# Performance work log

Measured on AMD Instinct MI355X. Metric: run time of the kernel, lower is better.

## Reference

```python
import jax, jax.numpy as jnp
import numpy as np

B, NC, N, DN, ALPHA = 8, 64, 128, 64, 2
HS, HM, HMOD = 256, 256, 64
STATE_IN, MSG_IN = 3 * DN, 2 * DN
MOD_IN = 2 * DN + 5
MOD_OUT = N * N + N


def _u(key, shape, fan_in):
    # kaiming_uniform-like init
    bound = 1.0 / np.sqrt(fan_in)
    return jax.random.uniform(key, shape, jnp.float32, -bound, bound)


def setup_inputs() -> dict:
    key = jax.random.key(0)
    ks = jax.random.split(key, 24)
    f = jnp.float32
    return {
        'h': jax.random.normal(ks[0], (B, NC, N, DN), f) * 0.01,
        'msg': jax.random.normal(ks[1], (B, NC, N, DN), f) * 0.01,
        'W': jax.random.normal(ks[2], (B, NC, N, N), f) * 0.05,
        'decay_logit': jnp.zeros((B, NC, N), f),
        'readout_drift': jnp.zeros((B, NC, 1), f),
        's_mem_live': jnp.zeros((B,), f),
        's_mem_ema_fast': jnp.zeros((B,), f),
        'H_aug_t': jax.random.normal(ks[3], (B, NC * DN), f),
        'neuron_id': jax.random.normal(ks[4], (NC, N, DN), f) * 0.02,
        'state_w1': _u(ks[5], (HS, STATE_IN), STATE_IN),
        'state_b1': jnp.zeros((HS,), f),
        'state_w2': _u(ks[6], (DN, HS), HS) * 0.1,
        'state_b2': jnp.zeros((DN,), f),
        'msg_w1': _u(ks[7], (HM, MSG_IN), MSG_IN),
        'msg_b1': jnp.zeros((HM,), f),
        'msg_w2': _u(ks[8], (DN, HM), HM) * 0.1,
        'msg_b2': jnp.zeros((DN,), f),
        'inject_w': _u(ks[9], (NC, ALPHA * DN, DN), DN),
        'inject_b': jnp.zeros((NC, ALPHA * DN), f),
        'mod_w1': _u(ks[10], (NC, MOD_IN, HMOD), HMOD),
        'mod_b1': jnp.zeros((NC, HMOD), f),
        'mod_w2': _u(ks[11], (NC, HMOD, MOD_OUT), MOD_OUT) * 0.01,
        'mod_b2': jnp.zeros((NC, MOD_OUT), f),
    }


def _mlp2(x, w1, b1, w2, b2):
    # F.linear -> tanh -> F.linear -> tanh
    hid = jnp.tanh(jnp.einsum('...i,hi->...h', x, w1) + b1)
    return jnp.tanh(jnp.einsum('...h,oh->...o', hid, w2) + b2)


def reference(h, msg, W, decay_logit, readout_drift, s_mem_live, s_mem_ema_fast,
              H_aug_t, neuron_id, state_w1, state_b1, state_w2, state_b2,
              msg_w1, msg_b1, msg_w2, msg_b2, inject_w, inject_b,
              mod_w1, mod_b1, mod_w2, mod_b2):
    # --- message passing: received = W @ msg  [B,NC,N,DN] ---
    received = jnp.einsum('bcij,bcjd->bcid', W, msg)

    # --- inject external input into the first ALPHA (input) neurons ---
    cell_slice = H_aug_t.reshape(B, NC, DN)               # [B,NC,DN]
    inject = jnp.einsum('bni,noi->bno', cell_slice, inject_w) + inject_b[None]
    inject = inject.reshape(B, NC, ALPHA, DN)
    received = received.at[:, :, :ALPHA].add(inject)

    # --- state update MLP (shared across cells/neurons) ---
    nid = jnp.broadcast_to(neuron_id[None], (B, NC, N, DN))
    state_in = jnp.concatenate([h, received, nid], axis=-1)      # [B,NC,N,3*DN]
    h_new = _mlp2(state_in, state_w1, state_b1, state_w2, state_b2)

    # --- message MLP ---
    msg_in = jnp.concatenate([h_new, received], axis=-1)         # [B,NC,N,2*DN]
    msg_new = _mlp2(msg_in, msg_w1, msg_b1, msg_w2, msg_b2)

    # --- modulator input (per _build_mod_input) ---
    h_mean = h_new.mean(axis=2)                                  # [B,NC,DN]
    msg_mean = msg_new.mean(axis=2)                              # [B,NC,DN]
    W_stats = jnp.abs(W).mean(axis=-1).mean(axis=2, keepdims=True)  # [B,NC,1]
    decay_mean = decay_logit.mean(axis=2, keepdims=True)         # [B,NC,1]
    s1 = jnp.broadcast_to(s_mem_live[:, None, None], (B, NC, 1))
    s2 = jnp.broadcast_to(s_mem_ema_fast[:, None, None], (B, NC, 1))
    mod_input = jnp.concatenate(
        [h_mean, msg_mean, W_stats, decay_mean, readout_drift, s1, s2], axis=-1)

    # --- per-cell modulator MLP (per _modulator_forward) ---
    hidden = jnp.tanh(jnp.einsum('bni,nih->bnh', mod_input, mod_w1) + mod_b1[None])
    mod_out = jnp.einsum('bnh,nho->bno', hidden, mod_w2) + mod_b2[None]

    # --- apply modulator action to recurrent adjacency + decay ---
    delta_W = mod_out[..., :N * N].reshape(B, NC, N, N)
    delta_decay = mod_out[..., N * N:N * N + N].reshape(B, NC, N)
    W_new = W + delta_W
    decay_new = decay_logit + delta_decay
    return (h_new, msg_new, W_new, decay_new)
```

## Files before the change

### kernel.cpp

```cpp
#include <hip/hip_runtime.h>
#include <hip/hip_bf16.h>
#include <math.h>


typedef __bf16 bf16_t;
typedef __attribute__((ext_vector_type(8))) __bf16 bf16x8;
typedef __attribute__((ext_vector_type(4))) float f32x4;

__device__ __forceinline__ float fast_tanh(float x) {
  float e = __expf(2.0f * x);
  return 1.0f - 2.0f / (e + 1.0f);
}

__device__ __forceinline__ f32x4 mfma16(bf16x8 a, bf16x8 b, f32x4 c) {
  return __builtin_amdgcn_mfma_f32_16x16x32_bf16(a, b, c, 0, 0, 0);
}

__device__ __forceinline__ bf16x8 ldcvt8(const float* p) {
  f32x4 a = *(const f32x4*)p;
  f32x4 b = *(const f32x4*)(p + 4);
  bf16x8 o;
#pragma unroll
  for (int u = 0; u < 4; ++u) { o[u] = (bf16_t)a[u]; o[u + 4] = (bf16_t)b[u]; }
  return o;
}

__global__ __launch_bounds__(256) void k_convert(
    const float* __restrict__ sw1, const float* __restrict__ sw2,
    const float* __restrict__ mw1, const float* __restrict__ mw2,
    bf16_t* __restrict__ out) {
  int i = blockIdx.x * 256 + threadIdx.x;
  float v;
  if (i < 49152) v = sw1[i];
  else if (i < 65536) v = sw2[i - 49152];
  else if (i < 98304) v = mw1[i - 65536];
  else v = mw2[i - 98304];
  out[i] = (bf16_t)v;
}

__global__ __launch_bounds__(256) void k_fused(
    const float* __restrict__ W, const float* __restrict__ msg,
    const float* __restrict__ h, const float* __restrict__ nid,
    const float* __restrict__ Haug, const float* __restrict__ injw,
    const float* __restrict__ injb, const bf16_t* __restrict__ wbf,
    const float* __restrict__ sb1, const float* __restrict__ sb2,
    const float* __restrict__ msb1, const float* __restrict__ msb2,
    const float* __restrict__ decay, const float* __restrict__ rdrift,
    const float* __restrict__ sml, const float* __restrict__ smf,
    const float* __restrict__ mw1, const float* __restrict__ mb1,
    float* __restrict__ out_h, float* __restrict__ out_m,
    float* __restrict__ hidden) {
  int bc = blockIdx.x, c = bc & 63, b = bc >> 6;
  __shared__ bf16_t Mt[64][136];
  __shared__ bf16_t recs[128][72];
  __shared__ bf16_t hs[128][72];
  __shared__ bf16_t hnew[128][72];
  __shared__ float inj[128];
  __shared__ float hsum[4][64];
  __shared__ float msum[4][64];
  __shared__ float wsum[4];
  __shared__ float modin[133];
  int t = threadIdx.x;

  const float* Mp = msg + (size_t)bc * 8192;
  for (int s = 0; s < 8; ++s) {
    int e = (s * 256 + t) * 4;
    f32x4 v = *(const f32x4*)(Mp + e);
    int j = e >> 6, d = e & 63;
#pragma unroll
    for (int u = 0; u < 4; ++u) Mt[d + u][j] = (bf16_t)v[u];
  }
  if (t < 128) {
    const float* cell = Haug + (size_t)b * 4096 + c * 64;
    const float* iw = injw + (size_t)c * 8192 + t * 64;
    float a = injb[c * 128 + t];
    for (int k = 0; k < 64; ++k) a += cell[k] * iw[k];
    inj[t] = a;
  }
  __syncthreads();

  int wave = t >> 6, l = t & 63, lr = l & 15, kg = l >> 4;
  int r0 = wave * 32;

  const float* Wp = W + (size_t)bc * 16384;
  float asum = 0.f;
  f32x4 racc[2][4] = {};
#pragma unroll
  for (int ks = 0; ks < 4; ++ks) {
    int kof = ks * 32 + kg * 8;
    const float* p0 = Wp + (size_t)(r0 + lr) * 128 + kof;
    const float* p1 = Wp + (size_t)(r0 + 16 + lr) * 128 + kof;
    f32x4 x0 = *(const f32x4*)p0, x1 = *(const f32x4*)(p0 + 4);
    f32x4 y0 = *(const f32x4*)p1, y1 = *(const f32x4*)(p1 + 4);
    bf16x8 a0, a1;
#pragma unroll
    for (int u = 0; u < 4; ++u) {
      a0[u] = (bf16_t)x0[u]; a0[u + 4] = (bf16_t)x1[u];
      a1[u] = (bf16_t)y0[u]; a1[u + 4] = (bf16_t)y1[u];
      asum += fabsf(x0[u]) + fabsf(x1[u]) + fabsf(y0[u]) + fabsf(y1[u]);
    }
#pragma unroll
    for (int ni = 0; ni < 4; ++ni) {
      bf16x8 bfr = *(const bf16x8*)&Mt[ni * 16 + lr][kof];
      racc[0][ni] = mfma16(a0, bfr, racc[0][ni]);
      racc[1][ni] = mfma16(a1, bfr, racc[1][ni]);
    }
  }
#pragma unroll
  for (int mi = 0; mi < 2; ++mi)
#pragma unroll
    for (int ni = 0; ni < 4; ++ni)
#pragma unroll
      for (int r = 0; r < 4; ++r) {
        int row = r0 + mi * 16 + kg * 4 + r, col = ni * 16 + lr;
        float v = racc[mi][ni][r];
        if (row < 2) v += inj[row * 64 + col];
        recs[row][col] = (bf16_t)v;
      }

  const float* hp = h + (size_t)bc * 8192;
  const float* np2 = nid + (size_t)c * 8192;
  bf16x8 aA[2][6];
#pragma unroll
  for (int mi = 0; mi < 2; ++mi) {
    int row = r0 + mi * 16 + lr;
#pragma unroll
    for (int ks = 0; ks < 6; ++ks) {
      int kof = ks * 32 + kg * 8;
      if (ks < 2)      aA[mi][ks] = ldcvt8(hp + (size_t)row * 64 + kof);
      else if (ks < 4) aA[mi][ks] = *(const bf16x8*)&recs[row][kof - 64];
      else             aA[mi][ks] = ldcvt8(np2 + (size_t)row * 64 + (kof - 128));
    }
  }
  const bf16_t* w1b = wbf;
  const bf16_t* w2b = wbf + 49152;
  const bf16_t* w3b = wbf + 65536;
  const bf16_t* w4b = wbf + 98304;
  f32x4 acc2[2][4] = {};
  for (int hc = 0; hc < 4; ++hc) {
    f32x4 a1[2][4] = {};
#pragma unroll
    for (int ks = 0; ks < 6; ++ks) {
      int kof = ks * 32 + kg * 8;
#pragma unroll
      for (int ni = 0; ni < 4; ++ni) {
        bf16x8 bfr = *(const bf16x8*)(w1b + (size_t)(hc * 64 + ni * 16 + lr) * 192 + kof);
        a1[0][ni] = mfma16(aA[0][ks], bfr, a1[0][ni]);
        a1[1][ni] = mfma16(aA[1][ks], bfr, a1[1][ni]);
      }
    }
#pragma unroll
    for (int mi = 0; mi < 2; ++mi)
#pragma unroll
      for (int ni = 0; ni < 4; ++ni) {
        float bias = sb1[hc * 64 + ni * 16 + lr];
#pragma unroll
        for (int r = 0; r < 4; ++r)
          hs[r0 + mi * 16 + kg * 4 + r][ni * 16 + lr] = (bf16_t)fast_tanh(a1[mi][ni][r] + bias);
      }
#pragma unroll
    for (int ks = 0; ks < 2; ++ks) {
      int kof = ks * 32 + kg * 8;
      bf16x8 af0 = *(const bf16x8*)&hs[r0 + lr][kof];
      bf16x8 af1 = *(const bf16x8*)&hs[r0 + 16 + lr][kof];
#pragma unroll
      for (int ni = 0; ni < 4; ++ni) {
        bf16x8 bfr = *(const bf16x8*)(w2b + (size_t)(ni * 16 + lr) * 256 + hc * 64 + kof);
        acc2[0][ni] = mfma16(af0, bfr, acc2[0][ni]);
        acc2[1][ni] = mfma16(af1, bfr, acc2[1][ni]);
      }
    }
  }
  float* ohp = out_h + (size_t)bc * 8192;
  float hpart[4] = {0.f, 0.f, 0.f, 0.f};
#pragma unroll
  for (int mi = 0; mi < 2; ++mi)
#pragma unroll
    for (int ni = 0; ni < 4; ++ni) {
      float bias = sb2[ni * 16 + lr];
#pragma unroll
      for (int r = 0; r < 4; ++r) {
        int row = r0 + mi * 16 + kg * 4 + r, col = ni * 16 + lr;
        float v = fast_tanh(acc2[mi][ni][r] + bias);
        ohp[row * 64 + col] = v;
        hnew[row][col] = (bf16_t)v;
        hpart[ni] += v;
      }
    }
#pragma unroll
  for (int ni = 0; ni < 4; ++ni) {
    float s = hpart[ni];
    s += __shfl_xor(s, 16);
    s += __shfl_xor(s, 32);
    if (l < 16) hsum[wave][ni * 16 + l] = s;
  }

  bf16x8 aB[2][4];
#pragma unroll
  for (int mi = 0; mi < 2; ++mi) {
    int row = r0 + mi * 16 + lr;
#pragma unroll
    for (int ks = 0; ks < 4; ++ks) {
      int kof = ks * 32 + kg * 8;
      if (ks < 2) aB[mi][ks] = *(const bf16x8*)&hnew[row][kof];
      else        aB[mi][ks] = *(const bf16x8*)&recs[row][kof - 64];
    }
  }
  f32x4 acc3[2][4] = {};
  for (int hc = 0; hc < 4; ++hc) {
    f32x4 g3[2][4] = {};
#pragma unroll
    for (int ks = 0; ks < 4; ++ks) {
      int kof = ks * 32 + kg * 8;
#pragma unroll
      for (int ni = 0; ni < 4; ++ni) {
        bf16x8 bfr = *(const bf16x8*)(w3b + (size_t)(hc * 64 + ni * 16 + lr) * 128 + kof);
        g3[0][ni] = mfma16(aB[0][ks], bfr, g3[0][ni]);
        g3[1][ni] = mfma16(aB[1][ks], bfr, g3[1][ni]);
      }
    }
#pragma unroll
    for (int mi = 0; mi < 2; ++mi)
#pragma unroll
      for (int ni = 0; ni < 4; ++ni) {
        float bias = msb1[hc * 64 + ni * 16 + lr];
#pragma unroll
        for (int r = 0; r < 4; ++r)
          hs[r0 + mi * 16 + kg * 4 + r][ni * 16 + lr] = (bf16_t)fast_tanh(g3[mi][ni][r] + bias);
      }
#pragma unroll
    for (int ks = 0; ks < 2; ++ks) {
      int kof = ks * 32 + kg * 8;
      bf16x8 af0 = *(const bf16x8*)&hs[r0 + lr][kof];
      bf16x8 af1 = *(const bf16x8*)&hs[r0 + 16 + lr][kof];
#pragma unroll
      for (int ni = 0; ni < 4; ++ni) {
        bf16x8 bfr = *(const bf16x8*)(w4b + (size_t)(ni * 16 + lr) * 256 + hc * 64 + kof);
        acc3[0][ni] = mfma16(af0, bfr, acc3[0][ni]);
        acc3[1][ni] = mfma16(af1, bfr, acc3[1][ni]);
      }
    }
  }
  float* omp = out_m + (size_t)bc * 8192;
  float mpart[4] = {0.f, 0.f, 0.f, 0.f};
#pragma unroll
  for (int mi = 0; mi < 2; ++mi)
#pragma unroll
    for (int ni = 0; ni < 4; ++ni) {
      float bias = msb2[ni * 16 + lr];
#pragma unroll
      for (int r = 0; r < 4; ++r) {
        int row = r0 + mi * 16 + kg * 4 + r, col = ni * 16 + lr;
        float v = fast_tanh(acc3[mi][ni][r] + bias);
        omp[row * 64 + col] = v;
        mpart[ni] += v;
      }
    }
#pragma unroll
  for (int ni = 0; ni < 4; ++ni) {
    float s = mpart[ni];
    s += __shfl_xor(s, 16);
    s += __shfl_xor(s, 32);
    if (l < 16) msum[wave][ni * 16 + l] = s;
  }
  {
    float s = asum;
#pragma unroll
    for (int off = 32; off > 0; off >>= 1) s += __shfl_xor(s, off);
    if (l == 0) wsum[wave] = s;
  }
  if (wave == 3) {
    float s = decay[(size_t)bc * 128 + l] + decay[(size_t)bc * 128 + 64 + l];
#pragma unroll
    for (int off = 32; off > 0; off >>= 1) s += __shfl_xor(s, off);
    if (l == 0) modin[129] = s * (1.f / 128.f);
  }
  __syncthreads();

  if (t < 64)
    modin[t] = (hsum[0][t] + hsum[1][t] + hsum[2][t] + hsum[3][t]) * (1.f / 128.f);
  else if (t < 128) {
    int d = t - 64;
    modin[64 + d] = (msum[0][d] + msum[1][d] + msum[2][d] + msum[3][d]) * (1.f / 128.f);
  } else if (t == 128)
    modin[128] = (wsum[0] + wsum[1] + wsum[2] + wsum[3]) * (1.f / 16384.f);
  else if (t == 130) modin[130] = rdrift[bc];
  else if (t == 131) modin[131] = sml[b];
  else if (t == 132) modin[132] = smf[b];
  __syncthreads();

  if (t < 64) {
    const float* w = mw1 + (size_t)c * 133 * 64;
    float a = mb1[c * 64 + t];
    for (int i = 0; i < 133; ++i) a += modin[i] * w[i * 64 + t];
    hidden[((size_t)(c * 64 + t)) * 8 + b] = fast_tanh(a);
  }
}

__global__ __launch_bounds__(256) void k_apply(
    const float* __restrict__ hidden, const float* __restrict__ mw2,
    const float* __restrict__ mb2, const float* __restrict__ W,
    const float* __restrict__ decay, float* __restrict__ out_W,
    float* __restrict__ out_d) {
  int c = blockIdx.y, ch = blockIdx.x, t = threadIdx.x;
  int o = ch * 1024 + t * 4;
  if (o >= 16512) return;
  const float* w2 = mw2 + (size_t)c * 64 * 16512 + o;
  const float* hq = hidden + (size_t)c * 512;
  f32x4 bias = *(const f32x4*)(mb2 + (size_t)c * 16512 + o);
  f32x4 acc[8];
#pragma unroll
  for (int b = 0; b < 8; ++b) acc[b] = bias;
  for (int hh = 0; hh < 64; ++hh) {
    f32x4 wv = __builtin_nontemporal_load((const f32x4*)(w2 + (size_t)hh * 16512));
    f32x4 h0 = *(const f32x4*)(hq + hh * 8);
    f32x4 h1 = *(const f32x4*)(hq + hh * 8 + 4);
#pragma unroll
    for (int b = 0; b < 4; ++b) { acc[b] += h0[b] * wv; acc[b + 4] += h1[b] * wv; }
  }
  if (o < 16384) {
#pragma unroll
    for (int b = 0; b < 8; ++b) {
      size_t idx = (size_t)(b * 64 + c) * 16384 + o;
      f32x4 wv = *(const f32x4*)(W + idx);
      __builtin_nontemporal_store(wv + acc[b], (f32x4*)(out_W + idx));
    }
  } else {
    int i = o - 16384;
#pragma unroll
    for (int b = 0; b < 8; ++b) {
      size_t idx = (size_t)(b * 64 + c) * 128 + i;
      f32x4 dv = *(const f32x4*)(decay + idx);
      __builtin_nontemporal_store(dv + acc[b], (f32x4*)(out_d + idx));
    }
  }
}

extern "C" void kernel_launch(void* const* d_in, const int* in_sizes, int n_in,
                              void* d_out, int out_size, void* d_ws, size_t ws_size,
                              hipStream_t stream) {
  const float* h = (const float*)d_in[0];
  const float* msg = (const float*)d_in[1];
  const float* W = (const float*)d_in[2];
  const float* decay = (const float*)d_in[3];
  const float* rdrift = (const float*)d_in[4];
  const float* sml = (const float*)d_in[5];
  const float* smf = (const float*)d_in[6];
  const float* Haug = (const float*)d_in[7];
  const float* nid = (const float*)d_in[8];
  const float* sw1 = (const float*)d_in[9];
  const float* sb1 = (const float*)d_in[10];
  const float* sw2 = (const float*)d_in[11];
  const float* sb2 = (const float*)d_in[12];
  const float* mw1 = (const float*)d_in[13];
  const float* mb1 = (const float*)d_in[14];
  const float* mw2 = (const float*)d_in[15];
  const float* mb2 = (const float*)d_in[16];
  const float* injw = (const float*)d_in[17];
  const float* injb = (const float*)d_in[18];
  const float* modw1 = (const float*)d_in[19];
  const float* modb1 = (const float*)d_in[20];
  const float* modw2 = (const float*)d_in[21];
  const float* modb2 = (const float*)d_in[22];

  float* out = (float*)d_out;
  float* out_h = out;
  float* out_m = out + 4194304;
  float* out_W = out + 8388608;
  float* out_d = out + 16777216;

  char* wsb = (char*)d_ws;
  bf16_t* wbf = (bf16_t*)wsb;
  float* hidden = (float*)(wsb + 262144);

  k_convert<<<448, 256, 0, stream>>>(sw1, sw2, mw1, mw2, wbf);
  k_fused<<<512, 256, 0, stream>>>(W, msg, h, nid, Haug, injw, injb, wbf,
                                   sb1, sb2, mb1, mb2, decay, rdrift, sml, smf,
                                   modw1, modb1, out_h, out_m, hidden);
  k_apply<<<dim3(17, 64), 256, 0, stream>>>(hidden, modw2, modb2, W, decay, out_W, out_d);
}
```

Baseline: 535.1 us.

## Split fused kernel rows across eight waves and stage modulator hidden in LDS

The fused per-cell kernel now runs 512 threads in eight waves, each owning 16 rows instead of 32. This halves the accumulators per wave and should allow more waves in flight to hide latency. The h, neuron_id and decay loads are hoisted above the first barrier, and the inject dot product is vectorised. The apply kernel stages the per-cell hidden vector in shared memory rather than rereading it from global memory on every iteration. The cost is that each wave now fetches the bf16 MLP weights for only 16 rows, so weight traffic per MFMA roughly doubles.

Result: slower. 561.0 us (+4.8%).

```diff
diff --git a/kernel.cpp b/kernel.cpp
--- a/kernel.cpp
+++ b/kernel.cpp
@@ -38,7 +38,7 @@
   out[i] = (bf16_t)v;
 }
 
-__global__ __launch_bounds__(256) void k_fused(
+__global__ __launch_bounds__(512, 4) void k_fused(
     const float* __restrict__ W, const float* __restrict__ msg,
     const float* __restrict__ h, const float* __restrict__ nid,
     const float* __restrict__ Haug, const float* __restrict__ injw,
@@ -56,15 +56,17 @@
   __shared__ bf16_t hs[128][72];
   __shared__ bf16_t hnew[128][72];
   __shared__ float inj[128];
-  __shared__ float hsum[4][64];
-  __shared__ float msum[4][64];
-  __shared__ float wsum[4];
+  __shared__ float hsum[8][64];
+  __shared__ float msum[8][64];
+  __shared__ float wsum[8];
   __shared__ float modin[133];
   int t = threadIdx.x;
+  int wave = t >> 6, l = t & 63, lr = l & 15, kg = l >> 4;
+  int r0 = wave * 16;
 
   const float* Mp = msg + (size_t)bc * 8192;
-  for (int s = 0; s < 8; ++s) {
-    int e = (s * 256 + t) * 4;
+  for (int s = 0; s < 4; ++s) {
+    int e = (s * 512 + t) * 4;
     f32x4 v = *(const f32x4*)(Mp + e);
     int j = e >> 6, d = e & 63;
 #pragma unroll
@@ -74,119 +76,108 @@
     const float* cell = Haug + (size_t)b * 4096 + c * 64;
     const float* iw = injw + (size_t)c * 8192 + t * 64;
     float a = injb[c * 128 + t];
-    for (int k = 0; k < 64; ++k) a += cell[k] * iw[k];
+    for (int k = 0; k < 64; k += 4) {
+      f32x4 w4 = *(const f32x4*)(iw + k);
+      a += cell[k] * w4[0] + cell[k + 1] * w4[1] + cell[k + 2] * w4[2] + cell[k + 3] * w4[3];
+    }
     inj[t] = a;
   }
+
+  const float* hp = h + (size_t)bc * 8192;
+  const float* np2 = nid + (size_t)c * 8192;
+  int arow = r0 + lr;
+  bf16x8 aA[6];
+  aA[0] = ldcvt8(hp + (size_t)arow * 64 + kg * 8);
+  aA[1] = ldcvt8(hp + (size_t)arow * 64 + 32 + kg * 8);
+  aA[4] = ldcvt8(np2 + (size_t)arow * 64 + kg * 8);
+  aA[5] = ldcvt8(np2 + (size_t)arow * 64 + 32 + kg * 8);
+  float dv0 = 0.f, dv1 = 0.f;
+  if (wave == 7) {
+    dv0 = decay[(size_t)bc * 128 + l];
+    dv1 = decay[(size_t)bc * 128 + 64 + l];
+  }
   __syncthreads();
-
-  int wave = t >> 6, l = t & 63, lr = l & 15, kg = l >> 4;
-  int r0 = wave * 32;
 
   const float* Wp = W + (size_t)bc * 16384;
   float asum = 0.f;
-  f32x4 racc[2][4] = {};
+  f32x4 racc[4] = {};
 #pragma unroll
   for (int ks = 0; ks < 4; ++ks) {
     int kof = ks * 32 + kg * 8;
-    const float* p0 = Wp + (size_t)(r0 + lr) * 128 + kof;
-    const float* p1 = Wp + (size_t)(r0 + 16 + lr) * 128 + kof;
+    const float* p0 = Wp + (size_t)arow * 128 + kof;
     f32x4 x0 = *(const f32x4*)p0, x1 = *(const f32x4*)(p0 + 4);
-    f32x4 y0 = *(const f32x4*)p1, y1 = *(const f32x4*)(p1 + 4);
-    bf16x8 a0, a1;
+    bf16x8 a0;
 #pragma unroll
     for (int u = 0; u < 4; ++u) {
       a0[u] = (bf16_t)x0[u]; a0[u + 4] = (bf16_t)x1[u];
-      a1[u] = (bf16_t)y0[u]; a1[u + 4] = (bf16_t)y1[u];
-      asum += fabsf(x0[u]) + fabsf(x1[u]) + fabsf(y0[u]) + fabsf(y1[u]);
+      asum += fabsf(x0[u]) + fabsf(x1[u]);
     }
 #pragma unroll
     for (int ni = 0; ni < 4; ++ni) {
       bf16x8 bfr = *(const bf16x8*)&Mt[ni * 16 + lr][kof];
-      racc[0][ni] = mfma16(a0, bfr, racc[0][ni]);
-      racc[1][ni] = mfma16(a1, bfr, racc[1][ni]);
-    }
-  }
-#pragma unroll
-  for (int mi = 0; mi < 2; ++mi)
-#pragma unroll
-    for (int ni = 0; ni < 4; ++ni)
-#pragma unroll
-      for (int r = 0; r < 4; ++r) {
-        int row = r0 + mi * 16 + kg * 4 + r, col = ni * 16 + lr;
-        float v = racc[mi][ni][r];
-        if (row < 2) v += inj[row * 64 + col];
-        recs[row][col] = (bf16_t)v;
-      }
-
-  const float* hp = h + (size_t)bc * 8192;
-  const float* np2 = nid + (size_t)c * 8192;
-  bf16x8 aA[2][6];
-#pragma unroll
-  for (int mi = 0; mi < 2; ++mi) {
-    int row = r0 + mi * 16 + lr;
-#pragma unroll
-    for (int ks = 0; ks < 6; ++ks) {
-      int kof = ks * 32 + kg * 8;
-      if (ks < 2)      aA[mi][ks] = ldcvt8(hp + (size_t)row * 64 + kof);
-      else if (ks < 4) aA[mi][ks] = *(const bf16x8*)&recs[row][kof - 64];
-      else             aA[mi][ks] = ldcvt8(np2 + (size_t)row * 64 + (kof - 128));
-    }
-  }
+      racc[ni] = mfma16(a0, bfr, racc[ni]);
+    }
+  }
+#pragma unroll
+  for (int ni = 0; ni < 4; ++ni)
+#pragma unroll
+    for (int r = 0; r < 4; ++r) {
+      int row = r0 + kg * 4 + r, col = ni * 16 + lr;
+      float v = racc[ni][r];
+      if (row < 2) v += inj[row * 64 + col];
+      recs[row][col] = (bf16_t)v;
+    }
+
+  aA[2] = *(const bf16x8*)&recs[arow][kg * 8];
+  aA[3] = *(const bf16x8*)&recs[arow][32 + kg * 8];
   const bf16_t* w1b = wbf;
   const bf16_t* w2b = wbf + 49152;
   const bf16_t* w3b = wbf + 65536;
   const bf16_t* w4b = wbf + 98304;
-  f32x4 acc2[2][4] = {};
+  f32x4 acc2[4] = {};
   for (int hc = 0; hc < 4; ++hc) {
-    f32x4 a1[2][4] = {};
+    f32x4 a1[4] = {};
 #pragma unroll
     for (int ks = 0; ks < 6; ++ks) {
       int kof = ks * 32 + kg * 8;
 #pragma unroll
       for (int ni = 0; ni < 4; ++ni) {
         bf16x8 bfr = *(const bf16x8*)(w1b + (size_t)(hc * 64 + ni * 16 + lr) * 192 + kof);
-        a1[0][ni] = mfma16(aA[0][ks], bfr, a1[0][ni]);
-        a1[1][ni] = mfma16(aA[1][ks], bfr, a1[1][ni]);
+        a1[ni] = mfma16(aA[ks], bfr, a1[ni]);
       }
     }
 #pragma unroll
-    for (int mi = 0; mi < 2; ++mi)
-#pragma unroll
-      for (int ni = 0; ni < 4; ++ni) {
-        float bias = sb1[hc * 64 + ni * 16 + lr];
-#pragma unroll
-        for (int r = 0; r < 4; ++r)
-          hs[r0 + mi * 16 + kg * 4 + r][ni * 16 + lr] = (bf16_t)fast_tanh(a1[mi][ni][r] + bias);
-      }
+    for (int ni = 0; ni < 4; ++ni) {
+      float bias = sb1[hc * 64 + ni * 16 + lr];
+#pragma unroll
+      for (int r = 0; r < 4; ++r)
+        hs[r0 + kg * 4 + r][ni * 16 + lr] = (bf16_t)fast_tanh(a1[ni][r] + bias);
+    }
 #pragma unroll
     for (int ks = 0; ks < 2; ++ks) {
       int kof = ks * 32 + kg * 8;
-      bf16x8 af0 = *(const bf16x8*)&hs[r0 + lr][kof];
-      bf16x8 af1 = *(const bf16x8*)&hs[r0 + 16 + lr][kof];
+      bf16x8 af = *(const bf16x8*)&hs[arow][kof];
 #pragma unroll
       for (int ni = 0; ni < 4; ++ni) {
         bf16x8 bfr = *(const bf16x8*)(w2b + (size_t)(ni * 16 + lr) * 256 + hc * 64 + kof);
-        acc2[0][ni] = mfma16(af0, bfr, acc2[0][ni]);
-        acc2[1][ni] = mfma16(af1, bfr, acc2[1][ni]);
+        acc2[ni] = mfma16(af, bfr, acc2[ni]);
       }
     }
   }
   float* ohp = out_h + (size_t)bc * 8192;
   float hpart[4] = {0.f, 0.f, 0.f, 0.f};
 #pragma unroll
-  for (int mi = 0; mi < 2; ++mi)
-#pragma unroll
-    for (int ni = 0; ni < 4; ++ni) {
-      float bias = sb2[ni * 16 + lr];
-#pragma unroll
-      for (int r = 0; r < 4; ++r) {
-        int row = r0 + mi * 16 + kg * 4 + r, col = ni * 16 + lr;
-        float v = fast_tanh(acc2[mi][ni][r] + bias);
-        ohp[row * 64 + col] = v;
-        hnew[row][col] = (bf16_t)v;
-        hpart[ni] += v;
-      }
-    }
+  for (int ni = 0; ni < 4; ++ni) {
+    float bias = sb2[ni * 16 + lr];
+#pragma unroll
+    for (int r = 0; r < 4; ++r) {
+      int row = r0 + kg * 4 + r, col = ni * 16 + lr;
+      float v = fast_tanh(acc2[ni][r] + bias);
+      ohp[row * 64 + col] = v;
+      hnew[row][col] = (bf16_t)v;
+      hpart[ni] += v;
+    }
+  }
 #pragma unroll
   for (int ni = 0; ni < 4; ++ni) {
     float s = hpart[ni];
@@ -195,67 +186,54 @@
     if (l < 16) hsum[wave][ni * 16 + l] = s;
   }
 
-  bf16x8 aB[2][4];
-#pragma unroll
-  for (int mi = 0; mi < 2; ++mi) {
-    int row = r0 + mi * 16 + lr;
+  bf16x8 aB[4];
+  aB[0] = *(const bf16x8*)&hnew[arow][kg * 8];
+  aB[1] = *(const bf16x8*)&hnew[arow][32 + kg * 8];
+  aB[2] = aA[2];
+  aB[3] = aA[3];
+  f32x4 acc3[4] = {};
+  for (int hc = 0; hc < 4; ++hc) {
+    f32x4 g3[4] = {};
 #pragma unroll
     for (int ks = 0; ks < 4; ++ks) {
       int kof = ks * 32 + kg * 8;
-      if (ks < 2) aB[mi][ks] = *(const bf16x8*)&hnew[row][kof];
-      else        aB[mi][ks] = *(const bf16x8*)&recs[row][kof - 64];
-    }
-  }
-  f32x4 acc3[2][4] = {};
-  for (int hc = 0; hc < 4; ++hc) {
-    f32x4 g3[2][4] = {};
-#pragma unroll
-    for (int ks = 0; ks < 4; ++ks) {
-      int kof = ks * 32 + kg * 8;
 #pragma unroll
       for (int ni = 0; ni < 4; ++ni) {
         bf16x8 bfr = *(const bf16x8*)(w3b + (size_t)(hc * 64 + ni * 16 + lr) * 128 + kof);
-        g3[0][ni] = mfma16(aB[0][ks], bfr, g3[0][ni]);
-        g3[1][ni] = mfma16(aB[1][ks], bfr, g3[1][ni]);
+        g3[ni] = mfma16(aB[ks], bfr, g3[ni]);
       }
     }
 #pragma unroll
-    for (int mi = 0; mi < 2; ++mi)
-#pragma unroll
-      for (int ni = 0; ni < 4; ++ni) {
-        float bias = msb1[hc * 64 + ni * 16 + lr];
-#pragma unroll
-        for (int r = 0; r < 4; ++r)
-          hs[r0 + mi * 16 + kg * 4 + r][ni * 16 + lr] = (bf16_t)fast_tanh(g3[mi][ni][r] + bias);
-      }
+    for (int ni = 0; ni < 4; ++ni) {
+      float bias = msb1[hc * 64 + ni * 16 + lr];
+#pragma unroll
+      for (int r = 0; r < 4; ++r)
+        hs[r0 + kg * 4 + r][ni * 16 + lr] = (bf16_t)fast_tanh(g3[ni][r] + bias);
+    }
 #pragma unroll
     for (int ks = 0; ks < 2; ++ks) {
       int kof = ks * 32 + kg * 8;
-      bf16x8 af0 = *(const bf16x8*)&hs[r0 + lr][kof];
-      bf16x8 af1 = *(const bf16x8*)&hs[r0 + 16 + lr][kof];
+      bf16x8 af = *(const bf16x8*)&hs[arow][kof];
 #pragma unroll
       for (int ni = 0; ni < 4; ++ni) {
         bf16x8 bfr = *(const bf16x8*)(w4b + (size_t)(ni * 16 + lr) * 256 + hc * 64 + kof);
-        acc3[0][ni] = mfma16(af0, bfr, acc3[0][ni]);
-        acc3[1][ni] = mfma16(af1, bfr, acc3[1][ni]);
+        acc3[ni] = mfma16(af, bfr, acc3[ni]);
       }
     }
   }
   float* omp = out_m + (size_t)bc * 8192;
   float mpart[4] = {0.f, 0.f, 0.f, 0.f};
 #pragma unroll
-  for (int mi = 0; mi < 2; ++mi)
-#pragma unroll
-    for (int ni = 0; ni < 4; ++ni) {
-      float bias = msb2[ni * 16 + lr];
-#pragma unroll
-      for (int r = 0; r < 4; ++r) {
-        int row = r0 + mi * 16 + kg * 4 + r, col = ni * 16 + lr;
-        float v = fast_tanh(acc3[mi][ni][r] + bias);
-        omp[row * 64 + col] = v;
-        mpart[ni] += v;
-      }
-    }
+  for (int ni = 0; ni < 4; ++ni) {
+    float bias = msb2[ni * 16 + lr];
+#pragma unroll
+    for (int r = 0; r < 4; ++r) {
+      int row = r0 + kg * 4 + r, col = ni * 16 + lr;
+      float v = fast_tanh(acc3[ni][r] + bias);
+      omp[row * 64 + col] = v;
+      mpart[ni] += v;
+    }
+  }
 #pragma unroll
   for (int ni = 0; ni < 4; ++ni) {
     float s = mpart[ni];
@@ -269,22 +247,31 @@
     for (int off = 32; off > 0; off >>= 1) s += __shfl_xor(s, off);
     if (l == 0) wsum[wave] = s;
   }
-  if (wave == 3) {
-    float s = decay[(size_t)bc * 128 + l] + decay[(size_t)bc * 128 + 64 + l];
+  if (wave == 7) {
+    float s = dv0 + dv1;
 #pragma unroll
     for (int off = 32; off > 0; off >>= 1) s += __shfl_xor(s, off);
     if (l == 0) modin[129] = s * (1.f / 128.f);
   }
   __syncthreads();
 
-  if (t < 64)
-    modin[t] = (hsum[0][t] + hsum[1][t] + hsum[2][t] + hsum[3][t]) * (1.f / 128.f);
-  else if (t < 128) {
+  if (t < 64) {
+    float s = 0.f;
+#pragma unroll
+    for (int w = 0; w < 8; ++w) s += hsum[w][t];
+    modin[t] = s * (1.f / 128.f);
+  } else if (t < 128) {
     int d = t - 64;
-    modin[64 + d] = (msum[0][d] + msum[1][d] + msum[2][d] + msum[3][d]) * (1.f / 128.f);
-  } else if (t == 128)
-    modin[128] = (wsum[0] + wsum[1] + wsum[2] + wsum[3]) * (1.f / 16384.f);
-  else if (t == 130) modin[130] = rdrift[bc];
+    float s = 0.f;
+#pragma unroll
+    for (int w = 0; w < 8; ++w) s += msum[w][d];
+    modin[64 + d] = s * (1.f / 128.f);
+  } else if (t == 128) {
+    float s = 0.f;
+#pragma unroll
+    for (int w = 0; w < 8; ++w) s += wsum[w];
+    modin[128] = s * (1.f / 16384.f);
+  } else if (t == 130) modin[130] = rdrift[bc];
   else if (t == 131) modin[131] = sml[b];
   else if (t == 132) modin[132] = smf[b];
   __syncthreads();
@@ -303,18 +290,22 @@
     const float* __restrict__ decay, float* __restrict__ out_W,
     float* __restrict__ out_d) {
   int c = blockIdx.y, ch = blockIdx.x, t = threadIdx.x;
+  __shared__ float hid[64][8];
+  const float* hq = hidden + (size_t)c * 512;
+  ((float*)hid)[t] = hq[t];
+  ((float*)hid)[t + 256] = hq[t + 256];
+  __syncthreads();
   int o = ch * 1024 + t * 4;
   if (o >= 16512) return;
   const float* w2 = mw2 + (size_t)c * 64 * 16512 + o;
-  const float* hq = hidden + (size_t)c * 512;
   f32x4 bias = *(const f32x4*)(mb2 + (size_t)c * 16512 + o);
   f32x4 acc[8];
 #pragma unroll
   for (int b = 0; b < 8; ++b) acc[b] = bias;
   for (int hh = 0; hh < 64; ++hh) {
     f32x4 wv = __builtin_nontemporal_load((const f32x4*)(w2 + (size_t)hh * 16512));
-    f32x4 h0 = *(const f32x4*)(hq + hh * 8);
-    f32x4 h1 = *(const f32x4*)(hq + hh * 8 + 4);
+    f32x4 h0 = *(const f32x4*)&hid[hh][0];
+    f32x4 h1 = *(const f32x4*)&hid[hh][4];
 #pragma unroll
     for (int b = 0; b < 4; ++b) { acc[b] += h0[b] * wv; acc[b + 4] += h1[b] * wv; }
   }
@@ -374,7 +365,7 @@
   float* hidden = (float*)(wsb + 262144);
 
   k_convert<<<448, 256, 0, stream>>>(sw1, sw2, mw1, mw2, wbf);
-  k_fused<<<512, 256, 0, stream>>>(W, msg, h, nid, Haug, injw, injb, wbf,
+  k_fused<<<512, 512, 0, stream>>>(W, msg, h, nid, Haug, injw, injb, wbf,
                                    sb1, sb2, mb1, mb2, decay, rdrift, sml, smf,
                                    modw1, modb1, out_h, out_m, hidden);
   k_apply<<<dim3(17, 64), 256, 0, stream>>>(hidden, modw2, modb2, W, decay, out_W, out_d);
```
